# Kernel optimization log

Hardware: AMD Instinct MI355X
Metric: run time of the kernel (lower is better)

The kernel has to match this reference:

```python
import jax, jax.numpy as jnp
import numpy as np

B, S, DM1, DM2, DK, DV = 8, 2048, 768, 768, 64, 64
EPS = 1e-5


def setup_inputs() -> dict:
    key = jax.random.key(0)
    ks = jax.random.split(key, 8)
    s1 = 1.0 / np.sqrt(DM1)
    s2 = 1.0 / np.sqrt(DM2)
    return {
        "x_1": jax.random.normal(ks[0], (B, S, DM1), jnp.float32),
        "x_2": jax.random.normal(ks[1], (B, S, DM2), jnp.float32),
        "Wq": jax.random.uniform(ks[2], (DM1, DK), jnp.float32, -s1, s1),
        "bq": jnp.zeros((DK,), jnp.float32),
        "Wk": jax.random.uniform(ks[3], (DM2, DK), jnp.float32, -s2, s2),
        "bk": jnp.zeros((DK,), jnp.float32),
        "Wv": jax.random.uniform(ks[4], (DM2, DV), jnp.float32, -s2, s2),
        "bv": jnp.zeros((DV,), jnp.float32),
        "gamma": jnp.ones((DV,), jnp.float32),
        "beta": jnp.zeros((DV,), jnp.float32),
    }


def reference(x_1, x_2, Wq, bq, Wk, bk, Wv, bv, gamma, beta):
    q = jnp.einsum("bsd,dk->bsk", x_1, Wq) + bq            # [B,S,DK]
    k = jnp.einsum("bsd,dk->bsk", x_2, Wk) + bk            # [B,S,DK]
    v = jnp.einsum("bsd,dv->bsv", x_2, Wv) + bv            # [B,S,DV]
    scores = jnp.einsum("bqk,bsk->bqs", q, k) / jnp.sqrt(jnp.float32(DK))
    w = jax.nn.softmax(scores, axis=-1)                    # [B,S,S]
    # reverse-weight transform (reverse=True)
    dim = w.shape[1]
    w = (1.0 - w) / (dim - 1)
    attn = jnp.einsum("bqs,bsv->bqv", w, v)                # [B,S,DV]
    mu = jnp.mean(attn, axis=-1, keepdims=True)
    var = jnp.var(attn, axis=-1, keepdims=True)
    out = (attn - mu) * jax.lax.rsqrt(var + EPS) * gamma + beta
    return out
```

## Files before the change

kernel.cpp:

```cpp
#include <hip/hip_runtime.h>
#include <hip/hip_bf16.h>

#define BATCH 8
#define SEQ   2048
#define DM    768
#define DD    64
#define BS (BATCH * SEQ)
#define SCALEQ 0.1803369380478f

typedef __bf16 bf16x8 __attribute__((ext_vector_type(8)));
typedef float  f32x4  __attribute__((ext_vector_type(4)));
typedef short  short8 __attribute__((ext_vector_type(8)));
typedef short  short4v __attribute__((ext_vector_type(4)));

#define MFMA16(a, b, c) __builtin_amdgcn_mfma_f32_16x16x32_bf16((a), (b), (c), 0, 0, 0)

__device__ __forceinline__ short f2bf(float x) {
    unsigned u = __builtin_bit_cast(unsigned, x);
    u = (u + 0x7fffu + ((u >> 16) & 1u)) >> 16;
    return (short)u;
}
__device__ __forceinline__ float bf2f(short s) {
    unsigned u = ((unsigned)(unsigned short)s) << 16;
    return __builtin_bit_cast(float, u);
}
__device__ __forceinline__ bf16x8 cvt8(float4 a, float4 b) {
    bf16x8 r;
    r[0] = (__bf16)a.x; r[1] = (__bf16)a.y; r[2] = (__bf16)a.z; r[3] = (__bf16)a.w;
    r[4] = (__bf16)b.x; r[5] = (__bf16)b.y; r[6] = (__bf16)b.z; r[7] = (__bf16)b.w;
    return r;
}
__device__ __forceinline__ void glds16(const void* g, void* l) {
    __builtin_amdgcn_global_load_lds(
        (const __attribute__((address_space(1))) void*)g,
        (__attribute__((address_space(3))) void*)l, 16, 0, 0);
}

__global__ void prep_w_kernel(const float* __restrict__ Wq, const float* __restrict__ Wk,
                              const float* __restrict__ Wv, short* __restrict__ Wt,
                              float* __restrict__ C) {
    int idx = blockIdx.x * 256 + threadIdx.x;
    if (idx < BATCH * DD) C[idx] = 0.f;
    if (idx >= 3 * DM * DD) return;
    int m = idx / (DM * DD);
    int r = (idx % (DM * DD)) / DD;
    int c = idx % DD;
    const float* W = (m == 0) ? Wq : (m == 1) ? Wk : Wv;
    float scale = (m == 0) ? SCALEQ : 1.0f;
    Wt[m * DM * DD + c * DM + r] = f2bf(W[r * DD + c] * scale);
}

__global__ __launch_bounds__(256) void proj_kernel(
        const float* __restrict__ x1, const float* __restrict__ x2,
        const short* __restrict__ Wt,
        const float* __restrict__ bq, const float* __restrict__ bk,
        const float* __restrict__ bv,
        short* __restrict__ Qs, short* __restrict__ Kb, short* __restrict__ Vtb,
        float* __restrict__ C) {
    __shared__ __align__(16) short wl[2][2][64 * 64];
    const int tid = threadIdx.x, wave = tid >> 6, lane = tid & 63;
    const int quad = lane >> 4, l15 = lane & 15;
    const int kv = blockIdx.x & 1;
    const int r0 = (blockIdx.x >> 1) * 64;
    const float* x = kv ? x2 : x1;
    const short* W0 = Wt + (kv ? (size_t)(DM * DD) : 0);
    const short* W1 = Wt + 2 * (size_t)(DM * DD);

    const int wrow = lane >> 3;
    const int wpiece = ((lane & 7) ^ (lane >> 3)) * 8;

    const float* xp = x + (size_t)(r0 + wave * 16 + l15) * DM + quad * 8;

    f32x4 acc0[4] = {}, acc1[4] = {};

#pragma unroll
    for (int j = 0; j < 2; j++) {
        int rbase = wave * 16 + j * 8;
        glds16(W0 + (size_t)(rbase + wrow) * DM + wpiece, &wl[0][0][rbase * 64]);
        if (kv)
            glds16(W1 + (size_t)(rbase + wrow) * DM + wpiece, &wl[0][1][rbase * 64]);
    }
    float4 c0a = *(const float4*)(xp);
    float4 c0b = *(const float4*)(xp + 4);
    float4 c1a = *(const float4*)(xp + 32);
    float4 c1b = *(const float4*)(xp + 36);
    __syncthreads();

    const int swz = l15 & 7;
#pragma unroll
    for (int it = 0; it < 12; it++) {
        const int buf = it & 1;
        float4 n0a, n0b, n1a, n1b;
        if (it < 11) {
            const int k0 = (it + 1) * 64;
#pragma unroll
            for (int j = 0; j < 2; j++) {
                int rbase = wave * 16 + j * 8;
                glds16(W0 + (size_t)(rbase + wrow) * DM + k0 + wpiece,
                       &wl[buf ^ 1][0][rbase * 64]);
                if (kv)
                    glds16(W1 + (size_t)(rbase + wrow) * DM + k0 + wpiece,
                           &wl[buf ^ 1][1][rbase * 64]);
            }
            n0a = *(const float4*)(xp + k0);
            n0b = *(const float4*)(xp + k0 + 4);
            n1a = *(const float4*)(xp + k0 + 32);
            n1b = *(const float4*)(xp + k0 + 36);
        }
#pragma unroll
        for (int kc = 0; kc < 2; kc++) {
            bf16x8 af = cvt8(kc ? c1a : c0a, kc ? c1b : c0b);
#pragma unroll
            for (int tn = 0; tn < 4; tn++) {
                const int slot = ((kc * 4 + quad) ^ swz) * 8;
                bf16x8 b0 = *(const bf16x8*)&wl[buf][0][(tn * 16 + l15) * 64 + slot];
                acc0[tn] = MFMA16(af, b0, acc0[tn]);
                if (kv) {
                    bf16x8 b1 = *(const bf16x8*)&wl[buf][1][(tn * 16 + l15) * 64 + slot];
                    acc1[tn] = MFMA16(af, b1, acc1[tn]);
                }
            }
        }
        c0a = n0a; c0b = n0b; c1a = n1a; c1b = n1b;
        __syncthreads();
    }

    if (!kv) {
#pragma unroll
        for (int tn = 0; tn < 4; tn++) {
            int v = tn * 16 + l15;
            float bb = bq[v] * SCALEQ;
#pragma unroll
            for (int r = 0; r < 4; r++)
                Qs[(size_t)(r0 + wave * 16 + quad * 4 + r) * DD + v] = f2bf(acc0[tn][r] + bb);
        }
    } else {
#pragma unroll
        for (int tn = 0; tn < 4; tn++) {
            int v = tn * 16 + l15;
            float bb = bk[v];
#pragma unroll
            for (int r = 0; r < 4; r++)
                Kb[(size_t)(r0 + wave * 16 + quad * 4 + r) * DD + v] = f2bf(acc0[tn][r] + bb);
        }
        const int b = r0 / SEQ;
        const int sbase = (r0 % SEQ) + wave * 16 + quad * 4;
#pragma unroll
        for (int tn = 0; tn < 4; tn++) {
            int v = tn * 16 + l15;
            float bb = bv[v];
            short4v pk;
            float cs = 0.f;
#pragma unroll
            for (int r = 0; r < 4; r++) {
                pk[r] = f2bf(acc1[tn][r] + bb);
                cs += bf2f(pk[r]);
            }
            *(short4v*)(Vtb + ((size_t)b * DD + v) * SEQ + sbase) = pk;
            cs += __shfl_xor(cs, 16);
            cs += __shfl_xor(cs, 32);
            if (quad == 0) atomicAdd(&C[b * DD + v], cs);
        }
    }
}

#define PBS 72
__global__ __launch_bounds__(256, 2) void flash_kernel(
        const short* __restrict__ Q, const short* __restrict__ K,
        const short* __restrict__ Vt,
        short* __restrict__ Yp, float* __restrict__ Dp) {
    __shared__ __align__(16) short pbuf[4][64 * PBS];
    __shared__ float dl[4][64];
    const int tid  = threadIdx.x;
    const int wave = tid >> 6, lane = tid & 63, quad = lane >> 4, l15 = lane & 15;
    const int blk = blockIdx.x;
    const int b = blk & 7, qt = (blk >> 3) & 31, half = blk >> 8;
    const int q0 = qt * 64;

    bf16x8 qf[4][2];
#pragma unroll
    for (int qn = 0; qn < 4; qn++)
#pragma unroll
        for (int kc = 0; kc < 2; kc++)
            qf[qn][kc] = *(const bf16x8*)(Q + ((size_t)(b * SEQ + q0 + qn * 16 + l15)) * DD
                                          + kc * 32 + quad * 8);

    const short* Kbp = K  + (size_t)b * SEQ * DD;
    const short* Vbp = Vt + (size_t)b * DD * SEQ;
    f32x4 y[4][4] = {};
    float den[4] = {0.f, 0.f, 0.f, 0.f};
    short* pw = &pbuf[wave][0];

    const int s_begin = half * 1024 + wave * 256;
    for (int s0 = s_begin; s0 < s_begin + 256; s0 += 64) {
#pragma unroll
        for (int tn = 0; tn < 4; tn++) {
            const short* kf = Kbp + (size_t)(s0 + tn * 16 + l15) * DD + quad * 8;
            bf16x8 ka0 = *(const bf16x8*)kf;
            bf16x8 ka1 = *(const bf16x8*)(kf + 32);
#pragma unroll
            for (int qn = 0; qn < 4; qn++) {
                f32x4 z = {0.f, 0.f, 0.f, 0.f};
                z = MFMA16(ka0, qf[qn][0], z);
                z = MFMA16(ka1, qf[qn][1], z);
                short4v pk;
#pragma unroll
                for (int r = 0; r < 4; r++) {
                    float p = __builtin_amdgcn_exp2f(z[r]);
                    den[qn] += p;
                    pk[r] = f2bf(p);
                }
                *(short4v*)&pw[(qn * 16 + l15) * PBS + tn * 16 + quad * 4] = pk;
            }
        }
#pragma unroll
        for (int kc = 0; kc < 2; kc++) {
            bf16x8 pB[4];
#pragma unroll
            for (int qn = 0; qn < 4; qn++)
                pB[qn] = *(const bf16x8*)&pw[(qn * 16 + l15) * PBS + kc * 32 + quad * 8];
#pragma unroll
            for (int vn = 0; vn < 4; vn++) {
                bf16x8 va = *(const bf16x8*)(Vbp + (size_t)(vn * 16 + l15) * SEQ
                                             + s0 + kc * 32 + quad * 8);
#pragma unroll
                for (int qn = 0; qn < 4; qn++)
                    y[qn][vn] = MFMA16(va, pB[qn], y[qn][vn]);
            }
        }
    }
#pragma unroll
    for (int qn = 0; qn < 4; qn++) {
        den[qn] += __shfl_xor(den[qn], 16);
        den[qn] += __shfl_xor(den[qn], 32);
    }
#pragma unroll
    for (int qn = 0; qn < 4; qn++) {
#pragma unroll
        for (int vn = 0; vn < 4; vn++) {
            short4v pk;
#pragma unroll
            for (int r = 0; r < 4; r++) pk[r] = f2bf(y[qn][vn][r]);
            *(short4v*)&pw[(qn * 16 + l15) * PBS + vn * 16 + quad * 4] = pk;
        }
        if (quad == 0) dl[wave][qn * 16 + l15] = den[qn];
    }
    __syncthreads();
    {
        const int q = wave * 16 + l15;
        float D = dl[0][q] + dl[1][q] + dl[2][q] + dl[3][q];
        float ys[16];
#pragma unroll
        for (int j = 0; j < 16; j++) ys[j] = 0.f;
#pragma unroll
        for (int u = 0; u < 4; u++) {
#pragma unroll
            for (int h = 0; h < 2; h++) {
                bf16x8 t = *(const bf16x8*)&pbuf[u][q * PBS + quad * 16 + h * 8];
#pragma unroll
                for (int j = 0; j < 8; j++) ys[h * 8 + j] += (float)t[j];
            }
        }
        const size_t row = (size_t)b * SEQ + q0 + q;
        short8 o0, o1;
#pragma unroll
        for (int j = 0; j < 8; j++) { o0[j] = f2bf(ys[j]); o1[j] = f2bf(ys[8 + j]); }
        short* yout = Yp + ((size_t)half * BS + row) * DD + quad * 16;
        *(short8*)yout = o0;
        *(short8*)(yout + 8) = o1;
        if (quad == 0) Dp[half * BS + row] = D;
    }
}

__global__ __launch_bounds__(256) void reduce_ln_kernel(
        const short* __restrict__ Yp, const float* __restrict__ Dp,
        const float* __restrict__ C, const float* __restrict__ gamma,
        const float* __restrict__ beta, float* __restrict__ out) {
    const int row = blockIdx.x * 4 + (threadIdx.x >> 6);
    const int v = threadIdx.x & 63;
    const int b = row >> 11;
    float Y = bf2f(Yp[(size_t)row * DD + v]) + bf2f(Yp[((size_t)BS + row) * DD + v]);
    float D = Dp[row] + Dp[BS + row];
    float attn = (C[b * DD + v] - Y / D) * (1.0f / (float)(SEQ - 1));
    float msum = attn, ssum = attn * attn;
#pragma unroll
    for (int m = 1; m < 64; m <<= 1) {
        msum += __shfl_xor(msum, m);
        ssum += __shfl_xor(ssum, m);
    }
    float mu = msum * (1.0f / 64.0f);
    float var = ssum * (1.0f / 64.0f) - mu * mu;
    float rs = rsqrtf(var + 1e-5f);
    out[(size_t)row * DD + v] = (attn - mu) * rs * gamma[v] + beta[v];
}

extern "C" void kernel_launch(void* const* d_in, const int* in_sizes, int n_in,
                              void* d_out, int out_size, void* d_ws, size_t ws_size,
                              hipStream_t stream) {
    const float* x1    = (const float*)d_in[0];
    const float* x2    = (const float*)d_in[1];
    const float* Wq    = (const float*)d_in[2];
    const float* bq    = (const float*)d_in[3];
    const float* Wk    = (const float*)d_in[4];
    const float* bk    = (const float*)d_in[5];
    const float* Wv    = (const float*)d_in[6];
    const float* bv    = (const float*)d_in[7];
    const float* gamma = (const float*)d_in[8];
    const float* beta  = (const float*)d_in[9];
    float* out = (float*)d_out;

    char* ws = (char*)d_ws;
    short* Qs  = (short*)(ws);
    short* Kbf = (short*)(ws + (2ull << 20));
    short* Vtb = (short*)(ws + (4ull << 20));
    short* Wt  = (short*)(ws + (6ull << 20));
    float* Cc  = (float*)(ws + (6ull << 20) + 3 * DM * DD * 2);
    short* Yp  = (short*)(ws + (7ull << 20));
    float* Dp  = (float*)(ws + (11ull << 20));

    prep_w_kernel<<<576, 256, 0, stream>>>(Wq, Wk, Wv, Wt, Cc);
    proj_kernel<<<512, 256, 0, stream>>>(x1, x2, Wt, bq, bk, bv, Qs, Kbf, Vtb, Cc);
    flash_kernel<<<512, 256, 0, stream>>>(Qs, Kbf, Vtb, Yp, Dp);
    reduce_ln_kernel<<<BS / 4, 256, 0, stream>>>(Yp, Dp, Cc, gamma, beta, out);
}
```

Measured before the change: 171.5 us.

## Stage projection weights in larger padded LDS phases instead of double-buffered async loads

The projection kernel now stages weights in four 192-wide K phases, using plain register loads and a padded LDS row stride. This replaces the 64-wide double-buffered tiles that used global_load_lds with XOR swizzling. The aim is fewer barriers and larger staging chunks, with padding instead of swizzle to avoid bank conflicts. In exchange, weight loads no longer overlap compute within a phase, and x prefetch shrinks to one 32-wide step ahead.

Result: no change. 171.1 us (-0.2%).

```diff
diff --git a/kernel.cpp b/kernel.cpp
--- a/kernel.cpp
+++ b/kernel.cpp
@@ -29,11 +29,6 @@
     r[0] = (__bf16)a.x; r[1] = (__bf16)a.y; r[2] = (__bf16)a.z; r[3] = (__bf16)a.w;
     r[4] = (__bf16)b.x; r[5] = (__bf16)b.y; r[6] = (__bf16)b.z; r[7] = (__bf16)b.w;
     return r;
-}
-__device__ __forceinline__ void glds16(const void* g, void* l) {
-    __builtin_amdgcn_global_load_lds(
-        (const __attribute__((address_space(1))) void*)g,
-        (__attribute__((address_space(3))) void*)l, 16, 0, 0);
 }
 
 __global__ void prep_w_kernel(const float* __restrict__ Wq, const float* __restrict__ Wk,
@@ -50,6 +45,8 @@
     Wt[m * DM * DD + c * DM + r] = f2bf(W[r * DD + c] * scale);
 }
 
+#define PHK 192
+#define RSTR 200
 __global__ __launch_bounds__(256) void proj_kernel(
         const float* __restrict__ x1, const float* __restrict__ x2,
         const short* __restrict__ Wt,
@@ -57,7 +54,7 @@
         const float* __restrict__ bv,
         short* __restrict__ Qs, short* __restrict__ Kb, short* __restrict__ Vtb,
         float* __restrict__ C) {
-    __shared__ __align__(16) short wl[2][2][64 * 64];
+    __shared__ __align__(16) short wls[2][64 * RSTR];
     const int tid = threadIdx.x, wave = tid >> 6, lane = tid & 63;
     const int quad = lane >> 4, l15 = lane & 15;
     const int kv = blockIdx.x & 1;
@@ -66,62 +63,51 @@
     const short* W0 = Wt + (kv ? (size_t)(DM * DD) : 0);
     const short* W1 = Wt + 2 * (size_t)(DM * DD);
 
-    const int wrow = lane >> 3;
-    const int wpiece = ((lane & 7) ^ (lane >> 3)) * 8;
+    const int srow = tid >> 2;
+    const int skseg = tid & 3;
 
     const float* xp = x + (size_t)(r0 + wave * 16 + l15) * DM + quad * 8;
 
     f32x4 acc0[4] = {}, acc1[4] = {};
 
-#pragma unroll
-    for (int j = 0; j < 2; j++) {
-        int rbase = wave * 16 + j * 8;
-        glds16(W0 + (size_t)(rbase + wrow) * DM + wpiece, &wl[0][0][rbase * 64]);
-        if (kv)
-            glds16(W1 + (size_t)(rbase + wrow) * DM + wpiece, &wl[0][1][rbase * 64]);
-    }
-    float4 c0a = *(const float4*)(xp);
-    float4 c0b = *(const float4*)(xp + 4);
-    float4 c1a = *(const float4*)(xp + 32);
-    float4 c1b = *(const float4*)(xp + 36);
-    __syncthreads();
-
-    const int swz = l15 & 7;
-#pragma unroll
-    for (int it = 0; it < 12; it++) {
-        const int buf = it & 1;
-        float4 n0a, n0b, n1a, n1b;
-        if (it < 11) {
-            const int k0 = (it + 1) * 64;
-#pragma unroll
-            for (int j = 0; j < 2; j++) {
-                int rbase = wave * 16 + j * 8;
-                glds16(W0 + (size_t)(rbase + wrow) * DM + k0 + wpiece,
-                       &wl[buf ^ 1][0][rbase * 64]);
+    float4 cxa = *(const float4*)(xp);
+    float4 cxb = *(const float4*)(xp + 4);
+
+    for (int ph = 0; ph < 4; ph++) {
+        const int kbase = ph * PHK;
+#pragma unroll
+        for (int i = 0; i < 6; i++) {
+            int kp = skseg + 4 * i;
+            bf16x8 w = *(const bf16x8*)(W0 + (size_t)srow * DM + kbase + kp * 8);
+            *(bf16x8*)&wls[0][srow * RSTR + kp * 8] = w;
+        }
+        if (kv) {
+#pragma unroll
+            for (int i = 0; i < 6; i++) {
+                int kp = skseg + 4 * i;
+                bf16x8 w = *(const bf16x8*)(W1 + (size_t)srow * DM + kbase + kp * 8);
+                *(bf16x8*)&wls[1][srow * RSTR + kp * 8] = w;
+            }
+        }
+        __syncthreads();
+#pragma unroll
+        for (int st = 0; st < 6; st++) {
+            const int k0 = kbase + st * 32;
+            float4 nxa, nxb;
+            if (k0 + 32 < DM) {
+                nxa = *(const float4*)(xp + k0 + 32);
+                nxb = *(const float4*)(xp + k0 + 36);
+            }
+            bf16x8 af = cvt8(cxa, cxb);
+#pragma unroll
+            for (int tn = 0; tn < 4; tn++) {
+                const int lofs = (tn * 16 + l15) * RSTR + (st * 4 + quad) * 8;
+                acc0[tn] = MFMA16(af, *(const bf16x8*)&wls[0][lofs], acc0[tn]);
                 if (kv)
-                    glds16(W1 + (size_t)(rbase + wrow) * DM + k0 + wpiece,
-                           &wl[buf ^ 1][1][rbase * 64]);
-            }
-            n0a = *(const float4*)(xp + k0);
-            n0b = *(const float4*)(xp + k0 + 4);
-            n1a = *(const float4*)(xp + k0 + 32);
-            n1b = *(const float4*)(xp + k0 + 36);
-        }
-#pragma unroll
-        for (int kc = 0; kc < 2; kc++) {
-            bf16x8 af = cvt8(kc ? c1a : c0a, kc ? c1b : c0b);
-#pragma unroll
-            for (int tn = 0; tn < 4; tn++) {
-                const int slot = ((kc * 4 + quad) ^ swz) * 8;
-                bf16x8 b0 = *(const bf16x8*)&wl[buf][0][(tn * 16 + l15) * 64 + slot];
-                acc0[tn] = MFMA16(af, b0, acc0[tn]);
-                if (kv) {
-                    bf16x8 b1 = *(const bf16x8*)&wl[buf][1][(tn * 16 + l15) * 64 + slot];
-                    acc1[tn] = MFMA16(af, b1, acc1[tn]);
-                }
-            }
-        }
-        c0a = n0a; c0b = n0b; c1a = n1a; c1b = n1b;
+                    acc1[tn] = MFMA16(af, *(const bf16x8*)&wls[1][lofs], acc1[tn]);
+            }
+            cxa = nxa; cxb = nxb;
+        }
         __syncthreads();
     }
 
```
